# Performance work log

Measured on AMD Instinct MI355X. Metric: run time of the kernel, lower is better.

## Reference

```python
import jax, jax.numpy as jnp
import numpy as np

B, T, QS, KS, BN, DV = 32, 4096, 512, 512, 256, 512
TOPK = 20


def setup_inputs() -> dict:
    key = jax.random.key(0)
    ks = jax.random.split(key, 7)
    query = jax.random.normal(ks[0], (B, QS), jnp.float32)
    keys = jax.random.normal(ks[1], (B, T, KS), jnp.float32)
    values = jax.random.normal(ks[2], (B, T, DV), jnp.float32)
    masks = jax.random.bernoulli(ks[3], 0.1, (B, T))  # True = masked out
    W = jax.random.normal(ks[4], (BN, QS), jnp.float32) / np.float32(np.sqrt(QS))
    U = jax.random.normal(ks[5], (BN, KS), jnp.float32) / np.float32(np.sqrt(KS))
    b = jnp.ones((BN,), jnp.float32)
    w = jax.random.normal(ks[6], (1, BN), jnp.float32) / np.float32(np.sqrt(BN))
    return {"query": query, "keys": keys, "values": values,
            "W": W, "U": U, "b": b, "w": w, "masks": masks}


def reference(query, keys, values, W, U, b, w, masks):
    # Additive attention energies: w^T tanh(W q + U k + b)  -> [B, T, 1]
    Wh = query @ W.T                                   # [B, BN]
    Uv = jnp.einsum('btk,nk->btn', keys, U)            # [B, T, BN]
    energies = jnp.einsum('btn,on->bto', jnp.tanh(Wh[:, None, :] + Uv + b), w)
    energies = jnp.where(masks[:, :, None], -jnp.inf, energies)
    weights = jax.nn.softmax(energies, axis=1)         # [B, T, 1]
    dd = weights[..., 0]                               # [B, T]
    top_wei, idx = jax.lax.top_k(dd, TOPK)             # [B, TOPK]
    rows = jnp.arange(dd.shape[0])[:, None]
    res = jnp.zeros_like(dd).at[rows, idx].set(top_wei)  # sparsified weights
    res = jax.lax.stop_gradient(res)[..., None]        # .detach() in torch
    attn_feats = jnp.sum(values * res, axis=1)         # [B, DV]
    return attn_feats, weights, energies
```

## Files before the change

kernel.cpp:

```cpp
#include <hip/hip_runtime.h>
#include <hip/hip_bf16.h>
#include <math.h>

#define B_ 32
#define T_ 4096
#define QS_ 512
#define KS_ 512
#define BN_ 256
#define DV_ 512
#define TOPK_ 20

#define NEG_BIG (-1e30f)

typedef __bf16 bf16x8 __attribute__((ext_vector_type(8)));
typedef float  f32x4  __attribute__((ext_vector_type(4)));

__device__ __forceinline__ float tanh_fast(float x) {
    float e = __expf(2.f * x);
    return 1.f - 2.f * __builtin_amdgcn_rcpf(e + 1.f);
}

__global__ void convert_U(const float* __restrict__ U, __bf16* __restrict__ Uh,
                          __bf16* __restrict__ Ul) {
    int i = blockIdx.x * 256 + threadIdx.x;
    if (i < BN_ * KS_) {
        float x = U[i];
        __bf16 h = (__bf16)x;
        Uh[i] = h;
        Ul[i] = (__bf16)(x - (float)h);
    }
}

__global__ __launch_bounds__(256) void compute_whb(const float* __restrict__ query,
                                                   const float* __restrict__ W,
                                                   const float* __restrict__ bias,
                                                   float* __restrict__ Whb) {
    __shared__ float q[QS_];
    int b = blockIdx.x;
    int n = threadIdx.x;
    for (int k = threadIdx.x; k < QS_; k += 256) q[k] = query[b * QS_ + k];
    __syncthreads();
    const float4* wr = (const float4*)(W + (size_t)n * QS_);
    float acc = 0.f;
    #pragma unroll 4
    for (int k4 = 0; k4 < QS_ / 4; ++k4) {
        float4 wv = wr[k4];
        float4 qv = *(const float4*)&q[k4 * 4];
        acc += wv.x * qv.x + wv.y * qv.y + wv.z * qv.z + wv.w * qv.w;
    }
    Whb[b * BN_ + n] = acc + bias[n];
}

#define LDP 40

__global__ __launch_bounds__(256, 2) void gemm_energy_mfma(
    const float* __restrict__ keys,
    const __bf16* __restrict__ Uh, const __bf16* __restrict__ Ul,
    const float* __restrict__ Whb, const float* __restrict__ wvec,
    const int* __restrict__ masks, float* __restrict__ energies)
{
    __shared__ __bf16 As_hi[128][LDP];
    __shared__ __bf16 As_lo[128][LDP];
    __shared__ __bf16 Bs_hi[BN_][LDP];
    __shared__ __bf16 Bs_lo[BN_][LDP];
    __shared__ float  whb_s[BN_];
    __shared__ float  wv_s[BN_];
    __shared__ float  red[128][2];

    const int tid = threadIdx.x;
    const int b  = blockIdx.x >> 5;
    const int t0 = (blockIdx.x & 31) * 128;
    const float* keyb = keys + ((size_t)b * T_ + t0) * (size_t)KS_;

    const int w   = tid >> 6;
    const int L   = tid & 63;
    const int q   = L >> 4;
    const int l16 = L & 15;
    const int wr  = (w >> 1) * 64;
    const int wc  = (w & 1) * 128;

    if (tid < BN_) {
        whb_s[tid] = Whb[b * BN_ + tid];
        wv_s[tid]  = wvec[tid];
    }

    f32x4 acc[4][8];
    #pragma unroll
    for (int rt = 0; rt < 4; ++rt)
        #pragma unroll
        for (int ct = 0; ct < 8; ++ct)
            acc[rt][ct] = (f32x4){0.f, 0.f, 0.f, 0.f};

    const int ar = tid >> 1;
    const int akq = (tid & 1) * 16;

    for (int kc = 0; kc < KS_ / 32; ++kc) {
        const int kb = kc * 32;
        {
            const float* src = keyb + (size_t)ar * KS_ + kb + akq;
            float4 f0 = *(const float4*)(src + 0);
            float4 f1 = *(const float4*)(src + 4);
            float4 f2 = *(const float4*)(src + 8);
            float4 f3 = *(const float4*)(src + 12);
            float v[16] = {f0.x,f0.y,f0.z,f0.w, f1.x,f1.y,f1.z,f1.w,
                           f2.x,f2.y,f2.z,f2.w, f3.x,f3.y,f3.z,f3.w};
            bf16x8 h0, h1, l0, l1;
            #pragma unroll
            for (int i = 0; i < 8; ++i) {
                __bf16 h = (__bf16)v[i];
                h0[i] = h; l0[i] = (__bf16)(v[i] - (float)h);
                __bf16 h2 = (__bf16)v[i + 8];
                h1[i] = h2; l1[i] = (__bf16)(v[i + 8] - (float)h2);
            }
            *(bf16x8*)&As_hi[ar][akq]     = h0;
            *(bf16x8*)&As_hi[ar][akq + 8] = h1;
            *(bf16x8*)&As_lo[ar][akq]     = l0;
            *(bf16x8*)&As_lo[ar][akq + 8] = l1;
        }
        {
            const bf16x8* sh = (const bf16x8*)(Uh + (size_t)tid * KS_ + kb);
            const bf16x8* sl = (const bf16x8*)(Ul + (size_t)tid * KS_ + kb);
            #pragma unroll
            for (int c = 0; c < 4; ++c) {
                *(bf16x8*)&Bs_hi[tid][c * 8] = sh[c];
                *(bf16x8*)&Bs_lo[tid][c * 8] = sl[c];
            }
        }
        __syncthreads();

        bf16x8 ah[4], al[4];
        #pragma unroll
        for (int rt = 0; rt < 4; ++rt) {
            ah[rt] = *(const bf16x8*)&As_hi[wr + rt * 16 + l16][q * 8];
            al[rt] = *(const bf16x8*)&As_lo[wr + rt * 16 + l16][q * 8];
        }
        #pragma unroll
        for (int ct = 0; ct < 8; ++ct) {
            bf16x8 bh = *(const bf16x8*)&Bs_hi[wc + ct * 16 + l16][q * 8];
            bf16x8 bl = *(const bf16x8*)&Bs_lo[wc + ct * 16 + l16][q * 8];
            #pragma unroll
            for (int rt = 0; rt < 4; ++rt) {
                acc[rt][ct] = __builtin_amdgcn_mfma_f32_16x16x32_bf16(ah[rt], bh, acc[rt][ct], 0, 0, 0);
                acc[rt][ct] = __builtin_amdgcn_mfma_f32_16x16x32_bf16(ah[rt], bl, acc[rt][ct], 0, 0, 0);
                acc[rt][ct] = __builtin_amdgcn_mfma_f32_16x16x32_bf16(al[rt], bh, acc[rt][ct], 0, 0, 0);
            }
        }
        __syncthreads();
    }

    #pragma unroll
    for (int rt = 0; rt < 4; ++rt) {
        #pragma unroll
        for (int r = 0; r < 4; ++r) {
            float part = 0.f;
            #pragma unroll
            for (int ct = 0; ct < 8; ++ct) {
                int n = wc + ct * 16 + l16;
                part += wv_s[n] * tanh_fast(whb_s[n] + acc[rt][ct][r]);
            }
            part += __shfl_xor(part, 1);
            part += __shfl_xor(part, 2);
            part += __shfl_xor(part, 4);
            part += __shfl_xor(part, 8);
            if (l16 == 0) red[wr + rt * 16 + q * 4 + r][w & 1] = part;
        }
    }
    __syncthreads();
    if (tid < 128) {
        int t = t0 + tid;
        float e = red[tid][0] + red[tid][1];
        energies[(size_t)b * T_ + t] = (masks[b * T_ + t] != 0) ? NEG_BIG : e;
    }
}

__global__ __launch_bounds__(256) void softmax_topk_gather(
    const float* __restrict__ energies, const float* __restrict__ values,
    float* __restrict__ weights, float* __restrict__ attn)
{
    __shared__ float sm[T_];
    __shared__ float wred[4];
    __shared__ int   wredi[4];
    __shared__ float topv[TOPK_];
    __shared__ int   topi[TOPK_];

    int b = blockIdx.x, tid = threadIdx.x;
    int lane = tid & 63, wave = tid >> 6;

    float lmax = -INFINITY;
    for (int t = tid; t < T_; t += 256) {
        float e = energies[b * T_ + t];
        sm[t] = e;
        lmax = fmaxf(lmax, e);
    }
    #pragma unroll
    for (int o = 32; o; o >>= 1) lmax = fmaxf(lmax, __shfl_down(lmax, o, 64));
    if (lane == 0) wred[wave] = lmax;
    __syncthreads();
    float bmax = fmaxf(fmaxf(wred[0], wred[1]), fmaxf(wred[2], wred[3]));
    __syncthreads();

    float lsum = 0.f;
    for (int t = tid; t < T_; t += 256) {
        float p = expf(sm[t] - bmax);
        lsum += p;
        sm[t] = p;
    }
    #pragma unroll
    for (int o = 32; o; o >>= 1) lsum += __shfl_down(lsum, o, 64);
    if (lane == 0) wred[wave] = lsum;
    __syncthreads();
    float inv = 1.f / (wred[0] + wred[1] + wred[2] + wred[3]);

    for (int t = tid; t < T_; t += 256) {
        float wt = sm[t] * inv;
        sm[t] = wt;
        weights[b * T_ + t] = wt;
    }
    __syncthreads();

    for (int j = 0; j < TOPK_; ++j) {
        float bv = -1.f; int bi = T_;
        for (int t = tid; t < T_; t += 256) {
            float v = sm[t];
            if (v > bv || (v == bv && t < bi)) { bv = v; bi = t; }
        }
        #pragma unroll
        for (int o = 32; o; o >>= 1) {
            float ov = __shfl_down(bv, o, 64);
            int   oi = __shfl_down(bi, o, 64);
            if (ov > bv || (ov == bv && oi < bi)) { bv = ov; bi = oi; }
        }
        __syncthreads();
        if (lane == 0) { wred[wave] = bv; wredi[wave] = bi; }
        __syncthreads();
        if (tid == 0) {
            float fv = -1.f; int fi = T_;
            #pragma unroll
            for (int qq = 0; qq < 4; qq++) {
                if (wred[qq] > fv || (wred[qq] == fv && wredi[qq] < fi)) { fv = wred[qq]; fi = wredi[qq]; }
            }
            topv[j] = fv; topi[j] = fi;
            sm[fi] = -1.f;
        }
        __syncthreads();
    }

    for (int dv = tid; dv < DV_; dv += 256) {
        float acc = 0.f;
        #pragma unroll
        for (int j = 0; j < TOPK_; j++)
            acc += values[((size_t)b * T_ + topi[j]) * DV_ + dv] * topv[j];
        attn[b * DV_ + dv] = acc;
    }
}

extern "C" void kernel_launch(void* const* d_in, const int* in_sizes, int n_in,
                              void* d_out, int out_size, void* d_ws, size_t ws_size,
                              hipStream_t stream) {
    const float* query  = (const float*)d_in[0];
    const float* keys   = (const float*)d_in[1];
    const float* values = (const float*)d_in[2];
    const float* W      = (const float*)d_in[3];
    const float* U      = (const float*)d_in[4];
    const float* bias   = (const float*)d_in[5];
    const float* wv     = (const float*)d_in[6];
    const int*   masks  = (const int*)d_in[7];

    float* out      = (float*)d_out;
    float* attn     = out;
    float* weights  = out + B_ * DV_;
    float* energies = out + B_ * DV_ + B_ * T_;

    float*  Whb = (float*)d_ws;
    __bf16* Uh  = (__bf16*)((char*)d_ws + 32768);
    __bf16* Ul  = (__bf16*)((char*)d_ws + 32768 + 262144);

    convert_U<<<(BN_ * KS_ + 255) / 256, 256, 0, stream>>>(U, Uh, Ul);
    compute_whb<<<B_, 256, 0, stream>>>(query, W, bias, Whb);
    gemm_energy_mfma<<<(B_ * T_) / 128, 256, 0, stream>>>(keys, Uh, Ul, Whb, wv, masks, energies);
    softmax_topk_gather<<<B_, 256, 0, stream>>>(energies, values, weights, attn);
}
```

Measured before the change: 603.6 us.

## Double-buffer GEMM tiles with register prefetch and use 512-thread blocks

The energy GEMM kernel now uses 512 threads (8 waves, each computing a 64x64 sub-tile) and double-buffered LDS. The next K-chunk's global loads are issued into registers before the MFMAs on the current chunk, which removes one barrier per iteration and overlaps memory latency with compute. The softmax/top-k kernel also moves to 512 threads. LDS use roughly doubles, which may limit occupancy, and the per-iteration top-k loops now have more waves to reduce across.

```diff
diff --git a/kernel.cpp b/kernel.cpp
--- a/kernel.cpp
+++ b/kernel.cpp
@@ -53,19 +53,19 @@
 
 #define LDP 40
 
-__global__ __launch_bounds__(256, 2) void gemm_energy_mfma(
+__global__ __launch_bounds__(512, 2) void gemm_energy_mfma(
     const float* __restrict__ keys,
     const __bf16* __restrict__ Uh, const __bf16* __restrict__ Ul,
     const float* __restrict__ Whb, const float* __restrict__ wvec,
     const int* __restrict__ masks, float* __restrict__ energies)
 {
-    __shared__ __bf16 As_hi[128][LDP];
-    __shared__ __bf16 As_lo[128][LDP];
-    __shared__ __bf16 Bs_hi[BN_][LDP];
-    __shared__ __bf16 Bs_lo[BN_][LDP];
+    __shared__ __bf16 As_hi[2][128][LDP];
+    __shared__ __bf16 As_lo[2][128][LDP];
+    __shared__ __bf16 Bs_hi[2][BN_][LDP];
+    __shared__ __bf16 Bs_lo[2][BN_][LDP];
     __shared__ float  whb_s[BN_];
     __shared__ float  wv_s[BN_];
-    __shared__ float  red[128][2];
+    __shared__ float  red[128][4];
 
     const int tid = threadIdx.x;
     const int b  = blockIdx.x >> 5;
@@ -76,77 +76,96 @@
     const int L   = tid & 63;
     const int q   = L >> 4;
     const int l16 = L & 15;
-    const int wr  = (w >> 1) * 64;
-    const int wc  = (w & 1) * 128;
+    const int wr  = (w >> 2) * 64;
+    const int wc  = (w & 3) * 64;
 
     if (tid < BN_) {
         whb_s[tid] = Whb[b * BN_ + tid];
         wv_s[tid]  = wvec[tid];
     }
 
-    f32x4 acc[4][8];
+    f32x4 acc[4][4];
     #pragma unroll
     for (int rt = 0; rt < 4; ++rt)
         #pragma unroll
-        for (int ct = 0; ct < 8; ++ct)
+        for (int ct = 0; ct < 4; ++ct)
             acc[rt][ct] = (f32x4){0.f, 0.f, 0.f, 0.f};
 
-    const int ar = tid >> 1;
-    const int akq = (tid & 1) * 16;
-
-    for (int kc = 0; kc < KS_ / 32; ++kc) {
-        const int kb = kc * 32;
-        {
-            const float* src = keyb + (size_t)ar * KS_ + kb + akq;
-            float4 f0 = *(const float4*)(src + 0);
-            float4 f1 = *(const float4*)(src + 4);
-            float4 f2 = *(const float4*)(src + 8);
-            float4 f3 = *(const float4*)(src + 12);
-            float v[16] = {f0.x,f0.y,f0.z,f0.w, f1.x,f1.y,f1.z,f1.w,
-                           f2.x,f2.y,f2.z,f2.w, f3.x,f3.y,f3.z,f3.w};
-            bf16x8 h0, h1, l0, l1;
-            #pragma unroll
-            for (int i = 0; i < 8; ++i) {
-                __bf16 h = (__bf16)v[i];
-                h0[i] = h; l0[i] = (__bf16)(v[i] - (float)h);
-                __bf16 h2 = (__bf16)v[i + 8];
-                h1[i] = h2; l1[i] = (__bf16)(v[i + 8] - (float)h2);
-            }
-            *(bf16x8*)&As_hi[ar][akq]     = h0;
-            *(bf16x8*)&As_hi[ar][akq + 8] = h1;
-            *(bf16x8*)&As_lo[ar][akq]     = l0;
-            *(bf16x8*)&As_lo[ar][akq + 8] = l1;
-        }
-        {
-            const bf16x8* sh = (const bf16x8*)(Uh + (size_t)tid * KS_ + kb);
-            const bf16x8* sl = (const bf16x8*)(Ul + (size_t)tid * KS_ + kb);
-            #pragma unroll
-            for (int c = 0; c < 4; ++c) {
-                *(bf16x8*)&Bs_hi[tid][c * 8] = sh[c];
-                *(bf16x8*)&Bs_lo[tid][c * 8] = sl[c];
-            }
-        }
+    const int ar  = tid >> 2;
+    const int aco = (tid & 3) * 8;
+    const int br  = tid >> 1;
+    const int bco = (tid & 1) * 16;
+
+    const float*  asrc  = keyb + (size_t)ar * KS_ + aco;
+    const __bf16* bsrch = Uh + (size_t)br * KS_ + bco;
+    const __bf16* bsrcl = Ul + (size_t)br * KS_ + bco;
+
+    float4 a0, a1;
+    bf16x8 rb0, rb1, rb2, rb3;
+
+#define LOADK(kb) do {                                         \
+        a0  = *(const float4*)(asrc + (kb));                   \
+        a1  = *(const float4*)(asrc + (kb) + 4);               \
+        rb0 = *(const bf16x8*)(bsrch + (kb));                  \
+        rb1 = *(const bf16x8*)(bsrch + (kb) + 8);              \
+        rb2 = *(const bf16x8*)(bsrcl + (kb));                  \
+        rb3 = *(const bf16x8*)(bsrcl + (kb) + 8);              \
+    } while (0)
+
+#define STOREK(bufi) do {                                      \
+        float v[8] = {a0.x, a0.y, a0.z, a0.w,                  \
+                      a1.x, a1.y, a1.z, a1.w};                 \
+        bf16x8 h, l;                                           \
+        _Pragma("unroll")                                      \
+        for (int i = 0; i < 8; ++i) {                          \
+            __bf16 hh = (__bf16)v[i];                          \
+            h[i] = hh;                                         \
+            l[i] = (__bf16)(v[i] - (float)hh);                 \
+        }                                                      \
+        *(bf16x8*)&As_hi[bufi][ar][aco]     = h;               \
+        *(bf16x8*)&As_lo[bufi][ar][aco]     = l;               \
+        *(bf16x8*)&Bs_hi[bufi][br][bco]     = rb0;             \
+        *(bf16x8*)&Bs_hi[bufi][br][bco + 8] = rb1;             \
+        *(bf16x8*)&Bs_lo[bufi][br][bco]     = rb2;             \
+        *(bf16x8*)&Bs_lo[bufi][br][bco + 8] = rb3;             \
+    } while (0)
+
+#define COMPUTE(bufi) do {                                                         \
+        bf16x8 ah[4], al[4];                                                       \
+        _Pragma("unroll")                                                          \
+        for (int rt = 0; rt < 4; ++rt) {                                           \
+            ah[rt] = *(const bf16x8*)&As_hi[bufi][wr + rt * 16 + l16][q * 8];      \
+            al[rt] = *(const bf16x8*)&As_lo[bufi][wr + rt * 16 + l16][q * 8];      \
+        }                                                                          \
+        _Pragma("unroll")                                                          \
+        for (int ct = 0; ct < 4; ++ct) {                                           \
+            bf16x8 bh = *(const bf16x8*)&Bs_hi[bufi][wc + ct * 16 + l16][q * 8];   \
+            bf16x8 bl = *(const bf16x8*)&Bs_lo[bufi][wc + ct * 16 + l16][q * 8];   \
+            _Pragma("unroll")                                                      \
+            for (int rt = 0; rt < 4; ++rt) {                                       \
+                acc[rt][ct] = __builtin_amdgcn_mfma_f32_16x16x32_bf16(ah[rt], bh, acc[rt][ct], 0, 0, 0); \
+                acc[rt][ct] = __builtin_amdgcn_mfma_f32_16x16x32_bf16(ah[rt], bl, acc[rt][ct], 0, 0, 0); \
+                acc[rt][ct] = __builtin_amdgcn_mfma_f32_16x16x32_bf16(al[rt], bh, acc[rt][ct], 0, 0, 0); \
+            }                                                                      \
+        }                                                                          \
+    } while (0)
+
+    LOADK(0);
+    STOREK(0);
+    int cur = 0;
+    for (int kc = 0; kc < 15; ++kc) {
         __syncthreads();
-
-        bf16x8 ah[4], al[4];
-        #pragma unroll
-        for (int rt = 0; rt < 4; ++rt) {
-            ah[rt] = *(const bf16x8*)&As_hi[wr + rt * 16 + l16][q * 8];
-            al[rt] = *(const bf16x8*)&As_lo[wr + rt * 16 + l16][q * 8];
-        }
-        #pragma unroll
-        for (int ct = 0; ct < 8; ++ct) {
-            bf16x8 bh = *(const bf16x8*)&Bs_hi[wc + ct * 16 + l16][q * 8];
-            bf16x8 bl = *(const bf16x8*)&Bs_lo[wc + ct * 16 + l16][q * 8];
-            #pragma unroll
-            for (int rt = 0; rt < 4; ++rt) {
-                acc[rt][ct] = __builtin_amdgcn_mfma_f32_16x16x32_bf16(ah[rt], bh, acc[rt][ct], 0, 0, 0);
-                acc[rt][ct] = __builtin_amdgcn_mfma_f32_16x16x32_bf16(ah[rt], bl, acc[rt][ct], 0, 0, 0);
-                acc[rt][ct] = __builtin_amdgcn_mfma_f32_16x16x32_bf16(al[rt], bh, acc[rt][ct], 0, 0, 0);
-            }
-        }
-        __syncthreads();
-    }
+        LOADK((kc + 1) * 32);
+        COMPUTE(cur);
+        STOREK(cur ^ 1);
+        cur ^= 1;
+    }
+    __syncthreads();
+    COMPUTE(cur);
+
+#undef LOADK
+#undef STOREK
+#undef COMPUTE
 
     #pragma unroll
     for (int rt = 0; rt < 4; ++rt) {
@@ -154,7 +173,7 @@
         for (int r = 0; r < 4; ++r) {
             float part = 0.f;
             #pragma unroll
-            for (int ct = 0; ct < 8; ++ct) {
+            for (int ct = 0; ct < 4; ++ct) {
                 int n = wc + ct * 16 + l16;
                 part += wv_s[n] * tanh_fast(whb_s[n] + acc[rt][ct][r]);
             }
@@ -162,24 +181,24 @@
             part += __shfl_xor(part, 2);
             part += __shfl_xor(part, 4);
             part += __shfl_xor(part, 8);
-            if (l16 == 0) red[wr + rt * 16 + q * 4 + r][w & 1] = part;
+            if (l16 == 0) red[wr + rt * 16 + q * 4 + r][w & 3] = part;
         }
     }
     __syncthreads();
     if (tid < 128) {
         int t = t0 + tid;
-        float e = red[tid][0] + red[tid][1];
+        float e = red[tid][0] + red[tid][1] + red[tid][2] + red[tid][3];
         energies[(size_t)b * T_ + t] = (masks[b * T_ + t] != 0) ? NEG_BIG : e;
     }
 }
 
-__global__ __launch_bounds__(256) void softmax_topk_gather(
+__global__ __launch_bounds__(512) void softmax_topk_gather(
     const float* __restrict__ energies, const float* __restrict__ values,
     float* __restrict__ weights, float* __restrict__ attn)
 {
     __shared__ float sm[T_];
-    __shared__ float wred[4];
-    __shared__ int   wredi[4];
+    __shared__ float wred[8];
+    __shared__ int   wredi[8];
     __shared__ float topv[TOPK_];
     __shared__ int   topi[TOPK_];
 
@@ -187,7 +206,7 @@
     int lane = tid & 63, wave = tid >> 6;
 
     float lmax = -INFINITY;
-    for (int t = tid; t < T_; t += 256) {
+    for (int t = tid; t < T_; t += 512) {
         float e = energies[b * T_ + t];
         sm[t] = e;
         lmax = fmaxf(lmax, e);
@@ -196,11 +215,13 @@
     for (int o = 32; o; o >>= 1) lmax = fmaxf(lmax, __shfl_down(lmax, o, 64));
     if (lane == 0) wred[wave] = lmax;
     __syncthreads();
-    float bmax = fmaxf(fmaxf(wred[0], wred[1]), fmaxf(wred[2], wred[3]));
+    float bmax = -INFINITY;
+    #pragma unroll
+    for (int i = 0; i < 8; ++i) bmax = fmaxf(bmax, wred[i]);
     __syncthreads();
 
     float lsum = 0.f;
-    for (int t = tid; t < T_; t += 256) {
+    for (int t = tid; t < T_; t += 512) {
         float p = expf(sm[t] - bmax);
         lsum += p;
         sm[t] = p;
@@ -209,9 +230,12 @@
     for (int o = 32; o; o >>= 1) lsum += __shfl_down(lsum, o, 64);
     if (lane == 0) wred[wave] = lsum;
     __syncthreads();
-    float inv = 1.f / (wred[0] + wred[1] + wred[2] + wred[3]);
-
-    for (int t = tid; t < T_; t += 256) {
+    float tot = 0.f;
+    #pragma unroll
+    for (int i = 0; i < 8; ++i) tot += wred[i];
+    float inv = 1.f / tot;
+
+    for (int t = tid; t < T_; t += 512) {
         float wt = sm[t] * inv;
         sm[t] = wt;
         weights[b * T_ + t] = wt;
@@ -220,7 +244,7 @@
 
     for (int j = 0; j < TOPK_; ++j) {
         float bv = -1.f; int bi = T_;
-        for (int t = tid; t < T_; t += 256) {
+        for (int t = tid; t < T_; t += 512) {
             float v = sm[t];
             if (v > bv || (v == bv && t < bi)) { bv = v; bi = t; }
         }
@@ -236,7 +260,7 @@
         if (tid == 0) {
             float fv = -1.f; int fi = T_;
             #pragma unroll
-            for (int qq = 0; qq < 4; qq++) {
+            for (int qq = 0; qq < 8; qq++) {
                 if (wred[qq] > fv || (wred[qq] == fv && wredi[qq] < fi)) { fv = wred[qq]; fi = wredi[qq]; }
             }
             topv[j] = fv; topi[j] = fi;
@@ -245,7 +269,7 @@
         __syncthreads();
     }
 
-    for (int dv = tid; dv < DV_; dv += 256) {
+    for (int dv = tid; dv < DV_; dv += 512) {
         float acc = 0.f;
         #pragma unroll
         for (int j = 0; j < TOPK_; j++)
@@ -277,6 +301,6 @@
 
     convert_U<<<(BN_ * KS_ + 255) / 256, 256, 0, stream>>>(U, Uh, Ul);
     compute_whb<<<B_, 256, 0, stream>>>(query, W, bias, Whb);
-    gemm_energy_mfma<<<(B_ * T_) / 128, 256, 0, stream>>>(keys, Uh, Ul, Whb, wv, masks, energies);
-    softmax_topk_gather<<<B_, 256, 0, stream>>>(energies, values, weights, attn);
-}
+    gemm_energy_mfma<<<(B_ * T_) / 128, 512, 0, stream>>>(keys, Uh, Ul, Whb, wv, masks, energies);
+    softmax_topk_gather<<<B_, 512, 0, stream>>>(energies, values, weights, attn);
+}
```

After: 614.9 us. Within noise of the previous version (+1.9%).

## Use direct global-to-LDS loads with XOR swizzle and register-resident two-level top-k

Applied to the files above, without the earlier changes.

The GEMM kernel now loads the bf16 U tiles straight into LDS with global_load_lds instead of going through registers. It drops the padded LDS rows in favour of an XOR-swizzled layout meant to avoid bank conflicts, and it issues the keys loads before the LDS writes. The softmax/top-k kernel moves to 512 threads and keeps the energies in registers. Each wave finds its own top-20 with shuffles and no block barriers, then one wave merges the 160 candidates, removing the 20 rounds of serialized block-wide reductions. The risks are swizzle/mapping correctness for the direct LDS loads and higher register pressure.

```diff
diff --git a/kernel.cpp b/kernel.cpp
--- a/kernel.cpp
+++ b/kernel.cpp
@@ -18,6 +18,12 @@
 __device__ __forceinline__ float tanh_fast(float x) {
     float e = __expf(2.f * x);
     return 1.f - 2.f * __builtin_amdgcn_rcpf(e + 1.f);
+}
+
+__device__ __forceinline__ void glds16(const void* g, void* l) {
+    __builtin_amdgcn_global_load_lds(
+        (const __attribute__((address_space(1))) void*)g,
+        (__attribute__((address_space(3))) void*)l, 16, 0, 0);
 }
 
 __global__ void convert_U(const float* __restrict__ U, __bf16* __restrict__ Uh,
@@ -51,7 +57,6 @@
     Whb[b * BN_ + n] = acc + bias[n];
 }
 
-#define LDP 40
 
 __global__ __launch_bounds__(256, 2) void gemm_energy_mfma(
     const float* __restrict__ keys,
@@ -59,10 +64,10 @@
     const float* __restrict__ Whb, const float* __restrict__ wvec,
     const int* __restrict__ masks, float* __restrict__ energies)
 {
-    __shared__ __bf16 As_hi[128][LDP];
-    __shared__ __bf16 As_lo[128][LDP];
-    __shared__ __bf16 Bs_hi[BN_][LDP];
-    __shared__ __bf16 Bs_lo[BN_][LDP];
+    __shared__ __bf16 As_hi[128][32];
+    __shared__ __bf16 As_lo[128][32];
+    __shared__ __bf16 Bs_hi[BN_][32];
+    __shared__ __bf16 Bs_lo[BN_][32];
     __shared__ float  whb_s[BN_];
     __shared__ float  wv_s[BN_];
     __shared__ float  red[128][2];
@@ -78,6 +83,7 @@
     const int l16 = L & 15;
     const int wr  = (w >> 1) * 64;
     const int wc  = (w & 1) * 128;
+    const int pq  = (q ^ ((l16 >> 1) & 3)) * 8;
 
     if (tid < BN_) {
         whb_s[tid] = Whb[b * BN_ + tid];
@@ -91,17 +97,33 @@
         for (int ct = 0; ct < 8; ++ct)
             acc[rt][ct] = (f32x4){0.f, 0.f, 0.f, 0.f};
 
-    const int ar = tid >> 1;
+    const int ar  = tid >> 1;
     const int akq = (tid & 1) * 16;
-
-    for (int kc = 0; kc < KS_ / 32; ++kc) {
+    const int xr  = (ar >> 1) & 3;
+    const int pa0 = (((tid & 1) * 2)     ^ xr) * 8;
+    const int pa1 = (((tid & 1) * 2 + 1) ^ xr) * 8;
+    const float* asrc = keyb + (size_t)ar * KS_ + akq;
+
+    const int brow0 = w * 64 + (L >> 2);
+    const int bcl   = ((L & 3) ^ ((L >> 3) & 3)) * 8;
+    const __bf16* bsh = Uh + (size_t)brow0 * KS_ + bcl;
+    const __bf16* bsl = Ul + (size_t)brow0 * KS_ + bcl;
+
+    for (int kc = 0; kc < 16; ++kc) {
         const int kb = kc * 32;
+
+        float4 f0 = *(const float4*)(asrc + kb + 0);
+        float4 f1 = *(const float4*)(asrc + kb + 4);
+        float4 f2 = *(const float4*)(asrc + kb + 8);
+        float4 f3 = *(const float4*)(asrc + kb + 12);
+
+        #pragma unroll
+        for (int j = 0; j < 4; ++j) {
+            glds16(bsh + kb + j * 16 * KS_, &Bs_hi[w * 64 + j * 16][0]);
+            glds16(bsl + kb + j * 16 * KS_, &Bs_lo[w * 64 + j * 16][0]);
+        }
+
         {
-            const float* src = keyb + (size_t)ar * KS_ + kb + akq;
-            float4 f0 = *(const float4*)(src + 0);
-            float4 f1 = *(const float4*)(src + 4);
-            float4 f2 = *(const float4*)(src + 8);
-            float4 f3 = *(const float4*)(src + 12);
             float v[16] = {f0.x,f0.y,f0.z,f0.w, f1.x,f1.y,f1.z,f1.w,
                            f2.x,f2.y,f2.z,f2.w, f3.x,f3.y,f3.z,f3.w};
             bf16x8 h0, h1, l0, l1;
@@ -112,32 +134,23 @@
                 __bf16 h2 = (__bf16)v[i + 8];
                 h1[i] = h2; l1[i] = (__bf16)(v[i + 8] - (float)h2);
             }
-            *(bf16x8*)&As_hi[ar][akq]     = h0;
-            *(bf16x8*)&As_hi[ar][akq + 8] = h1;
-            *(bf16x8*)&As_lo[ar][akq]     = l0;
-            *(bf16x8*)&As_lo[ar][akq + 8] = l1;
-        }
-        {
-            const bf16x8* sh = (const bf16x8*)(Uh + (size_t)tid * KS_ + kb);
-            const bf16x8* sl = (const bf16x8*)(Ul + (size_t)tid * KS_ + kb);
-            #pragma unroll
-            for (int c = 0; c < 4; ++c) {
-                *(bf16x8*)&Bs_hi[tid][c * 8] = sh[c];
-                *(bf16x8*)&Bs_lo[tid][c * 8] = sl[c];
-            }
+            *(bf16x8*)&As_hi[ar][pa0] = h0;
+            *(bf16x8*)&As_hi[ar][pa1] = h1;
+            *(bf16x8*)&As_lo[ar][pa0] = l0;
+            *(bf16x8*)&As_lo[ar][pa1] = l1;
         }
         __syncthreads();
 
         bf16x8 ah[4], al[4];
         #pragma unroll
         for (int rt = 0; rt < 4; ++rt) {
-            ah[rt] = *(const bf16x8*)&As_hi[wr + rt * 16 + l16][q * 8];
-            al[rt] = *(const bf16x8*)&As_lo[wr + rt * 16 + l16][q * 8];
+            ah[rt] = *(const bf16x8*)&As_hi[wr + rt * 16 + l16][pq];
+            al[rt] = *(const bf16x8*)&As_lo[wr + rt * 16 + l16][pq];
         }
         #pragma unroll
         for (int ct = 0; ct < 8; ++ct) {
-            bf16x8 bh = *(const bf16x8*)&Bs_hi[wc + ct * 16 + l16][q * 8];
-            bf16x8 bl = *(const bf16x8*)&Bs_lo[wc + ct * 16 + l16][q * 8];
+            bf16x8 bh = *(const bf16x8*)&Bs_hi[wc + ct * 16 + l16][pq];
+            bf16x8 bl = *(const bf16x8*)&Bs_lo[wc + ct * 16 + l16][pq];
             #pragma unroll
             for (int rt = 0; rt < 4; ++rt) {
                 acc[rt][ct] = __builtin_amdgcn_mfma_f32_16x16x32_bf16(ah[rt], bh, acc[rt][ct], 0, 0, 0);
@@ -173,79 +186,107 @@
     }
 }
 
-__global__ __launch_bounds__(256) void softmax_topk_gather(
+__global__ __launch_bounds__(512) void softmax_topk_gather(
     const float* __restrict__ energies, const float* __restrict__ values,
     float* __restrict__ weights, float* __restrict__ attn)
 {
-    __shared__ float sm[T_];
-    __shared__ float wred[4];
-    __shared__ int   wredi[4];
+    __shared__ float wred[8];
+    __shared__ float wtv[8][TOPK_];
+    __shared__ int   wti[8][TOPK_];
     __shared__ float topv[TOPK_];
     __shared__ int   topi[TOPK_];
 
     int b = blockIdx.x, tid = threadIdx.x;
     int lane = tid & 63, wave = tid >> 6;
 
+    float ev[8];
     float lmax = -INFINITY;
-    for (int t = tid; t < T_; t += 256) {
-        float e = energies[b * T_ + t];
-        sm[t] = e;
-        lmax = fmaxf(lmax, e);
-    }
-    #pragma unroll
-    for (int o = 32; o; o >>= 1) lmax = fmaxf(lmax, __shfl_down(lmax, o, 64));
+    #pragma unroll
+    for (int i = 0; i < 8; ++i) {
+        ev[i] = energies[b * T_ + tid + i * 512];
+        lmax = fmaxf(lmax, ev[i]);
+    }
+    #pragma unroll
+    for (int o = 32; o; o >>= 1) lmax = fmaxf(lmax, __shfl_xor(lmax, o, 64));
     if (lane == 0) wred[wave] = lmax;
     __syncthreads();
-    float bmax = fmaxf(fmaxf(wred[0], wred[1]), fmaxf(wred[2], wred[3]));
-    __syncthreads();
+    float bmax = -INFINITY;
+    #pragma unroll
+    for (int i = 0; i < 8; ++i) bmax = fmaxf(bmax, wred[i]);
 
     float lsum = 0.f;
-    for (int t = tid; t < T_; t += 256) {
-        float p = expf(sm[t] - bmax);
-        lsum += p;
-        sm[t] = p;
-    }
-    #pragma unroll
-    for (int o = 32; o; o >>= 1) lsum += __shfl_down(lsum, o, 64);
+    #pragma unroll
+    for (int i = 0; i < 8; ++i) {
+        ev[i] = expf(ev[i] - bmax);
+        lsum += ev[i];
+    }
+    #pragma unroll
+    for (int o = 32; o; o >>= 1) lsum += __shfl_xor(lsum, o, 64);
+    __syncthreads();
     if (lane == 0) wred[wave] = lsum;
     __syncthreads();
-    float inv = 1.f / (wred[0] + wred[1] + wred[2] + wred[3]);
-
-    for (int t = tid; t < T_; t += 256) {
-        float wt = sm[t] * inv;
-        sm[t] = wt;
-        weights[b * T_ + t] = wt;
-    }
-    __syncthreads();
+    float tot = 0.f;
+    #pragma unroll
+    for (int i = 0; i < 8; ++i) tot += wred[i];
+    float inv = 1.f / tot;
+
+    float lv[8]; int li[8];
+    #pragma unroll
+    for (int i = 0; i < 8; ++i) {
+        float wt = ev[i] * inv;
+        weights[b * T_ + tid + i * 512] = wt;
+        lv[i] = wt;
+        li[i] = tid + i * 512;
+    }
 
     for (int j = 0; j < TOPK_; ++j) {
         float bv = -1.f; int bi = T_;
-        for (int t = tid; t < T_; t += 256) {
-            float v = sm[t];
-            if (v > bv || (v == bv && t < bi)) { bv = v; bi = t; }
-        }
+        #pragma unroll
+        for (int i = 0; i < 8; ++i)
+            if (lv[i] > bv || (lv[i] == bv && li[i] < bi)) { bv = lv[i]; bi = li[i]; }
         #pragma unroll
         for (int o = 32; o; o >>= 1) {
-            float ov = __shfl_down(bv, o, 64);
-            int   oi = __shfl_down(bi, o, 64);
+            float ov = __shfl_xor(bv, o, 64);
+            int   oi = __shfl_xor(bi, o, 64);
             if (ov > bv || (ov == bv && oi < bi)) { bv = ov; bi = oi; }
         }
-        __syncthreads();
-        if (lane == 0) { wred[wave] = bv; wredi[wave] = bi; }
-        __syncthreads();
-        if (tid == 0) {
-            float fv = -1.f; int fi = T_;
-            #pragma unroll
-            for (int qq = 0; qq < 4; qq++) {
-                if (wred[qq] > fv || (wred[qq] == fv && wredi[qq] < fi)) { fv = wred[qq]; fi = wredi[qq]; }
+        if (lane == 0) { wtv[wave][j] = bv; wti[wave][j] = bi; }
+        #pragma unroll
+        for (int i = 0; i < 8; ++i)
+            if (li[i] == bi) lv[i] = -1.f;
+    }
+    __syncthreads();
+
+    if (wave == 0) {
+        float cv[3]; int ci[3];
+        #pragma unroll
+        for (int c = 0; c < 3; ++c) {
+            int idx = lane + c * 64;
+            if (idx < 8 * TOPK_) {
+                cv[c] = wtv[idx / TOPK_][idx % TOPK_];
+                ci[c] = wti[idx / TOPK_][idx % TOPK_];
+            } else { cv[c] = -2.f; ci[c] = T_ + 1; }
+        }
+        for (int j = 0; j < TOPK_; ++j) {
+            float bv = -2.f; int bi = T_ + 1;
+            #pragma unroll
+            for (int c = 0; c < 3; ++c)
+                if (cv[c] > bv || (cv[c] == bv && ci[c] < bi)) { bv = cv[c]; bi = ci[c]; }
+            #pragma unroll
+            for (int o = 32; o; o >>= 1) {
+                float ov = __shfl_xor(bv, o, 64);
+                int   oi = __shfl_xor(bi, o, 64);
+                if (ov > bv || (ov == bv && oi < bi)) { bv = ov; bi = oi; }
             }
-            topv[j] = fv; topi[j] = fi;
-            sm[fi] = -1.f;
-        }
-        __syncthreads();
-    }
-
-    for (int dv = tid; dv < DV_; dv += 256) {
+            if (lane == 0) { topv[j] = bv; topi[j] = bi; }
+            #pragma unroll
+            for (int c = 0; c < 3; ++c)
+                if (ci[c] == bi) cv[c] = -2.f;
+        }
+    }
+    __syncthreads();
+
+    for (int dv = tid; dv < DV_; dv += 512) {
         float acc = 0.f;
         #pragma unroll
         for (int j = 0; j < TOPK_; j++)
@@ -278,5 +319,5 @@
     convert_U<<<(BN_ * KS_ + 255) / 256, 256, 0, stream>>>(U, Uh, Ul);
     compute_whb<<<B_, 256, 0, stream>>>(query, W, bias, Whb);
     gemm_energy_mfma<<<(B_ * T_) / 128, 256, 0, stream>>>(keys, Uh, Ul, Whb, wv, masks, energies);
-    softmax_topk_gather<<<B_, 256, 0, stream>>>(energies, values, weights, attn);
-}
+    softmax_topk_gather<<<B_, 512, 0, stream>>>(energies, values, weights, attn);
+}
```

Result: faster. 554.6 us (-8.1%).
